# Optimization experiments

Hardware: AMD Instinct MI355X
Metric: run time of the kernel (lower is better)

The kernel has to match this reference:

```python
import jax, jax.numpy as jnp
import numpy as np

D = 128
K = 8
TEMPERATURE = 1.0
LN_EPS = 1e-5
NORM_EPS = 1e-12


def setup_inputs() -> dict:
    key = jax.random.key(0)
    ks = jax.random.split(key, 6)
    B = 262144
    global_prosody = jax.random.normal(ks[0], (B, D), dtype=jnp.float32)
    W = jax.random.normal(ks[1], (D, D), dtype=jnp.float32) / np.sqrt(D)
    b = jnp.zeros((D,), dtype=jnp.float32)
    gamma = jnp.ones((D,), dtype=jnp.float32)
    beta = jnp.zeros((D,), dtype=jnp.float32)
    # codebook initialized as rows of an orthonormal basis (SVD of random init)
    init = jax.random.normal(ks[2], (D, K), dtype=jnp.float32)
    U, _, _ = jnp.linalg.svd(init, full_matrices=False)
    codebook = U[:, :K].T  # (K, D)
    return {"global_prosody": global_prosody, "W": W, "b": b,
            "gamma": gamma, "beta": beta, "codebook": codebook}


def _l2norm(x, axis=-1):
    n = jnp.sqrt(jnp.sum(x * x, axis=axis, keepdims=True))
    return x / jnp.maximum(n, NORM_EPS)


def reference(global_prosody, W, b, gamma, beta, codebook):
    # proj: Linear + LayerNorm
    h = global_prosody @ W.T + b                      # (B, D)
    mu = jnp.mean(h, axis=-1, keepdims=True)
    var = jnp.var(h, axis=-1, keepdims=True)
    h = (h - mu) / jnp.sqrt(var + LN_EPS) * gamma + beta
    # cosine-sim logits
    h_norm = _l2norm(h)                               # (B, D)
    cb_norm = _l2norm(codebook)                       # (K, D)
    logits = (h_norm @ cb_norm.T) / TEMPERATURE       # (B, K)
    soft_assign = jax.nn.softmax(logits, axis=-1)
    hard_indices = jnp.argmax(logits, axis=-1)        # (B,)
    hard_assign = jax.nn.one_hot(hard_indices, K, dtype=jnp.float32)
    # straight-through assignment
    assign = hard_assign + soft_assign - jax.lax.stop_gradient(soft_assign)
    embedding = assign @ codebook                     # (B, D)
    return hard_indices, soft_assign, embedding, logits
```

## Files before the change

### kernel.cpp

```cpp
#include <hip/hip_runtime.h>
#include <math.h>

#define DD 128
#define KK 8
#define LN_EPS 1e-5f
#define NORM_EPS 1e-12f

typedef __attribute__((ext_vector_type(8))) short bf16x8;
typedef __attribute__((ext_vector_type(16))) float f32x16;
typedef unsigned int uint;
typedef unsigned short ushort;

#define G2B_OFF_F   (122880 / 4)
#define SCAL_OFF_F  (123904 / 4)

__device__ inline void split3(float x, uint& h, uint& m, uint& l) {
    uint u0 = __float_as_uint(x);
    uint rh = (u0 + 0x7FFFu + ((u0 >> 16) & 1u)) & 0xFFFF0000u;
    float xh = __uint_as_float(rh);
    float r1 = x - xh;
    uint u1 = __float_as_uint(r1);
    uint rm = (u1 + 0x7FFFu + ((u1 >> 16) & 1u)) & 0xFFFF0000u;
    float xm = __uint_as_float(rm);
    float r2 = r1 - xm;
    uint u2 = __float_as_uint(r2);
    uint rl = (u2 + 0x7FFFu + ((u2 >> 16) & 1u));
    h = rh; m = rm; l = rl;
}

__device__ inline void split3t(float x, uint& h, uint& m, uint& l) {
    uint u0 = __float_as_uint(x);
    float xh = __uint_as_float(u0 & 0xFFFF0000u);
    float r1 = x - xh;
    uint u1 = __float_as_uint(r1);
    float xm = __uint_as_float(u1 & 0xFFFF0000u);
    float r2 = r1 - xm;
    h = u0; m = u1; l = __float_as_uint(r2);
}

__device__ inline uint packhi(uint a1, uint a0) {
    return __builtin_amdgcn_perm(a1, a0, 0x07060302u);
}

__device__ inline void split2packt(float e0, float e1, uint& ph, uint& pm, uint& pl) {
    uint h0, m0, l0, h1, m1, l1;
    split3t(e0, h0, m0, l0);
    split3t(e1, h1, m1, l1);
    ph = packhi(h1, h0);
    pm = packhi(m1, m0);
    pl = packhi(l1, l0);
}

union FragU  { uint4 u; bf16x8 f; };
union AccU16 { f32x16 v; float a[16]; };

__global__ void l1q_prep0(const float* __restrict__ b, const float* __restrict__ gamma,
                          const float* __restrict__ beta, const float* __restrict__ cb,
                          float* __restrict__ ws)
{
    __shared__ float invn_s[KK];
    const int t = threadIdx.x;
    if (t < KK) {
        float s = 0.f;
        for (int j = 0; j < DD; ++j) { float v = cb[t * DD + j]; s = fmaf(v, v, s); }
        invn_s[t] = 1.0f / fmaxf(sqrtf(s), NORM_EPS);
    }
    __syncthreads();
    {
        float g = gamma[t];
        float* g2b = ws + G2B_OFF_F;
        g2b[2 * t]     = g * g;
        g2b[2 * t + 1] = b[t];
    }
    float* scal = ws + SCAL_OFF_F;
    if (t < KK) {
        float in = invn_s[t];
        float p = 0.f, q = 0.f, cu = 0.f;
        for (int j = 0; j < DD; ++j) {
            float c = cb[t * DD + j] * in;
            p  = fmaf(c, gamma[j], p);
            q  = fmaf(c, beta[j], q);
            cu = fmaf(c * gamma[j], b[j], cu);
        }
        scal[t]      = p;
        scal[8 + t]  = q;
        scal[22 + t] = cu;
    }
    if (t == 16) { float s = 0.f; for (int j = 0; j < DD; ++j) { float g = gamma[j]; s = fmaf(g, g, s); } scal[16] = s; }
    if (t == 17) { float s = 0.f; for (int j = 0; j < DD; ++j) s = fmaf(gamma[j], beta[j], s); scal[17] = s; }
    if (t == 18) { float s = 0.f; for (int j = 0; j < DD; ++j) { float v = beta[j]; s = fmaf(v, v, s); } scal[18] = s; }
    if (t == 19) { float s = 0.f; for (int j = 0; j < DD; ++j) s += b[j]; scal[19] = s; }
    if (t == 20) { float s = 0.f; for (int j = 0; j < DD; ++j) s = fmaf(gamma[j] * gamma[j], b[j], s); scal[20] = s; }
    if (t == 21) { float s = 0.f; for (int j = 0; j < DD; ++j) s = fmaf(gamma[j] * beta[j], b[j], s); scal[21] = s; }
}

__global__ void l1q_prepA(const float* __restrict__ W, const float* __restrict__ b,
                          const float* __restrict__ gamma, const float* __restrict__ beta,
                          const float* __restrict__ cb, ushort* __restrict__ wsA)
{
    __shared__ float invn_s[KK];
    __shared__ float we[11][DD];
    __shared__ float wext[32][16];
    const int t = threadIdx.x;
    const int jt = blockIdx.x >> 3;
    const int ks = blockIdx.x & 7;

    if (jt == 4) {
        if (t < KK) {
            float s = 0.f;
            for (int j = 0; j < DD; ++j) { float v = cb[t * DD + j]; s = fmaf(v, v, s); }
            invn_s[t] = 1.0f / fmaxf(sqrtf(s), NORM_EPS);
        }
        __syncthreads();
        for (int idx = t; idx < 11 * DD; idx += 256) {
            int e = idx / DD, j = idx % DD;
            float g = gamma[j];
            float v;
            if (e == 0)      v = 1.0f;
            else if (e == 1) v = g * g;
            else if (e == 2) v = g * beta[j];
            else             v = cb[(e - 3) * DD + j] * invn_s[e - 3] * g;
            we[e][j] = v;
        }
        __syncthreads();
    }

    for (int idx = t; idx < 512; idx += 256) {
        int jl = idx >> 4, kk = idx & 15;
        int k = ks * 16 + kk;
        float val;
        if (jt < 4) {
            val = W[(jt * 32 + jl) * DD + k];
        } else if (jl < 11) {
            float s = 0.f;
            for (int j = 0; j < DD; ++j) s = fmaf(we[jl][j], W[j * DD + k], s);
            val = s;
        } else {
            val = 0.f;
        }
        wext[jl][kk] = val;
    }
    __syncthreads();

    for (int idx = t; idx < 512; idx += 256) {
        int jl = idx >> 4, kk = idx & 15;
        int lane = jl + 32 * (kk >> 3);
        int i = kk & 7;
        uint h, m, l;
        split3(wext[jl][kk], h, m, l);
        int base = jt * 8 + ks;
        wsA[(0 * 40 + base) * 512 + lane * 8 + i] = (ushort)(h >> 16);
        wsA[(1 * 40 + base) * 512 + lane * 8 + i] = (ushort)(m >> 16);
        wsA[(2 * 40 + base) * 512 + lane * 8 + i] = (ushort)(l >> 16);
    }
}

__global__ __launch_bounds__(1024, 4)
void l1q_main(const float* __restrict__ x, const ushort* __restrict__ wsA,
              const float* __restrict__ wsf, const float* __restrict__ cb,
              float* __restrict__ out_idx, float* __restrict__ out_soft,
              float* __restrict__ out_emb, float* __restrict__ out_log,
              int B)
{
    __shared__ uint4 Wl4[7680];
    __shared__ float gath[16][352];
    __shared__ int   besti[16][32];
    __shared__ float g2b_s[256];
    __shared__ float scal_s[32];

    const int t = threadIdx.x;
    const int wave = t >> 6;
    const int lane = t & 63;
    const int n = lane & 31;
    const int h = lane >> 5;

    const float* xp = x + (size_t)(blockIdx.x * 1024 + wave * 32 + n) * DD + h * 8;
    float4 ra = *(const float4*)(xp + 0);
    float4 rc = *(const float4*)(xp + 4);

    {
        const uint4* src = (const uint4*)wsA;
        #pragma unroll
        for (int i = 0; i < 8; ++i) {
            int idx = t + i * 1024;
            if (idx < 7680) Wl4[idx] = src[idx];
        }
    }
    if (t < 256) g2b_s[t] = wsf[G2B_OFF_F + t];
    if (t < 32)  scal_s[t] = wsf[SCAL_OFF_F + t];
    __syncthreads();

    const float inv128 = 1.0f / 128.0f;

    #pragma unroll 1
    for (int c = 0; c < 2; ++c) {
        const int rowbase = blockIdx.x * 1024 + c * 512 + wave * 32;
        const float* xnext = (c == 0) ? (xp + 512 * DD) : xp;

        f32x16 acc[5];
        #pragma unroll
        for (int jt = 0; jt < 5; ++jt)
            #pragma unroll
            for (int r = 0; r < 16; ++r) acc[jt][r] = 0.f;

        #pragma unroll
        for (int ks = 0; ks < 8; ++ks) {
            const float* pf = (ks < 7) ? (xp + (ks + 1) * 16) : xnext;
            float4 na = *(const float4*)(pf + 0);
            float4 nc = *(const float4*)(pf + 4);

            FragU xh, xm, xl;
            split2packt(ra.x, ra.y, xh.u.x, xm.u.x, xl.u.x);
            split2packt(ra.z, ra.w, xh.u.y, xm.u.y, xl.u.y);
            split2packt(rc.x, rc.y, xh.u.z, xm.u.z, xl.u.z);
            split2packt(rc.z, rc.w, xh.u.w, xm.u.w, xl.u.w);

            __builtin_amdgcn_s_setprio(1);
            #pragma unroll
            for (int jt = 0; jt < 5; ++jt) {
                const int pl = jt * 8 + ks;
                FragU wh, wm, wl;
                wh.u = Wl4[(0 * 40 + pl) * 64 + lane];
                wm.u = Wl4[(1 * 40 + pl) * 64 + lane];
                wl.u = Wl4[(2 * 40 + pl) * 64 + lane];
                f32x16 cacc = acc[jt];
                cacc = __builtin_amdgcn_mfma_f32_32x32x16_bf16(wl.f, xh.f, cacc, 0, 0, 0);
                cacc = __builtin_amdgcn_mfma_f32_32x32x16_bf16(wh.f, xl.f, cacc, 0, 0, 0);
                cacc = __builtin_amdgcn_mfma_f32_32x32x16_bf16(wm.f, xm.f, cacc, 0, 0, 0);
                cacc = __builtin_amdgcn_mfma_f32_32x32x16_bf16(wm.f, xh.f, cacc, 0, 0, 0);
                cacc = __builtin_amdgcn_mfma_f32_32x32x16_bf16(wh.f, xm.f, cacc, 0, 0, 0);
                cacc = __builtin_amdgcn_mfma_f32_32x32x16_bf16(wh.f, xh.f, cacc, 0, 0, 0);
                acc[jt] = cacc;
            }
            __builtin_amdgcn_s_setprio(0);
            ra = na; rc = nc;
        }

        float s2a = 0.f, t2a = 0.f;
        #pragma unroll
        for (int jt = 0; jt < 4; ++jt) {
            AccU16 a; a.v = acc[jt];
            #pragma unroll
            for (int rq = 0; rq < 4; ++rq) {
                int jb = jt * 32 + 8 * rq + 4 * h;
                #pragma unroll
                for (int r = 0; r < 4; ++r) {
                    float2 gb = *(const float2*)&g2b_s[2 * (jb + r)];
                    float hv = a.a[rq * 4 + r] + gb.y;
                    float h2 = hv * hv;
                    s2a += h2;
                    t2a = fmaf(gb.x, h2, t2a);
                }
            }
        }
        s2a += __shfl_xor(s2a, 32);
        t2a += __shfl_xor(t2a, 32);

        {
            AccU16 a; a.v = acc[4];
            #pragma unroll
            for (int rq = 0; rq < 4; ++rq) {
                #pragma unroll
                for (int r = 0; r < 4; ++r) {
                    int local = r + 8 * rq + 4 * h;
                    if (local < 11) gath[wave][n * 11 + local] = a.a[rq * 4 + r];
                }
            }
        }
        __builtin_amdgcn_s_waitcnt(0);
        const float* gp = &gath[wave][n * 11];

        const float cg2s = scal_s[16], cgbs = scal_s[17], cb2s = scal_s[18];

        float s1  = gp[0] + scal_s[19];
        float t1  = gp[1] + scal_s[20];
        float r1v = gp[2] + scal_s[21];
        float u[KK];
        #pragma unroll
        for (int k = 0; k < KK; ++k) u[k] = gp[3 + k] + scal_s[22 + k];

        float mu = s1 * inv128;
        float var = fmaf(-mu, mu, s2a * inv128);
        float istd = 1.0f / sqrtf(var + LN_EPS);
        float nrm2 = istd * istd * (t2a - 2.f * mu * t1 + mu * mu * cg2s)
                   + 2.f * istd * (r1v - mu * cgbs) + cb2s;
        float rinv = 1.0f / fmaxf(sqrtf(fmaxf(nrm2, 0.f)), NORM_EPS);

        float lg[KK];
        #pragma unroll
        for (int k = 0; k < KK; ++k)
            lg[k] = (istd * (u[k] - mu * scal_s[k]) + scal_s[8 + k]) * rinv;

        float mx = lg[0]; int bi = 0;
        #pragma unroll
        for (int k = 1; k < KK; ++k) if (lg[k] > mx) { mx = lg[k]; bi = k; }

        float ex[KK], se = 0.f;
        #pragma unroll
        for (int k = 0; k < KK; ++k) { ex[k] = expf(lg[k] - mx); se += ex[k]; }
        float rse = 1.0f / se;

        const int m = rowbase + n;
        if (h == 0) {
            out_idx[m] = (float)bi;
            besti[wave][n] = bi;
            *(float4*)&out_log[(size_t)m * KK]     = make_float4(lg[0], lg[1], lg[2], lg[3]);
            *(float4*)&out_log[(size_t)m * KK + 4] = make_float4(lg[4], lg[5], lg[6], lg[7]);
        } else {
            *(float4*)&out_soft[(size_t)m * KK]     = make_float4(ex[0] * rse, ex[1] * rse, ex[2] * rse, ex[3] * rse);
            *(float4*)&out_soft[(size_t)m * KK + 4] = make_float4(ex[4] * rse, ex[5] * rse, ex[6] * rse, ex[7] * rse);
        }

        __builtin_amdgcn_s_waitcnt(0);
        const float4* cb4 = (const float4*)cb;
        float4* eo = (float4*)out_emb;
        #pragma unroll
        for (int i = 0; i < 16; ++i) {
            int f4 = lane + 64 * i;
            int rl = f4 >> 5;
            int cc = f4 & 31;
            int k0 = besti[wave][rl];
            eo[(size_t)(rowbase + rl) * 32 + cc] = cb4[k0 * 32 + cc];
        }

        xp = xnext;
    }
}

extern "C" void kernel_launch(void* const* d_in, const int* in_sizes, int n_in,
                              void* d_out, int out_size, void* d_ws, size_t ws_size,
                              hipStream_t stream) {
    const float* x     = (const float*)d_in[0];
    const float* W     = (const float*)d_in[1];
    const float* b     = (const float*)d_in[2];
    const float* gamma = (const float*)d_in[3];
    const float* beta  = (const float*)d_in[4];
    const float* cb    = (const float*)d_in[5];
    const int B = in_sizes[0] / DD;

    float*  ws  = (float*)d_ws;
    ushort* wsA = (ushort*)d_ws;

    float* out    = (float*)d_out;
    float* o_idx  = out;
    float* o_soft = out + (size_t)B;
    float* o_emb  = out + (size_t)B * (1 + KK);
    float* o_log  = out + (size_t)B * (1 + KK + DD);

    hipLaunchKernelGGL(l1q_prep0, dim3(1), dim3(128), 0, stream, b, gamma, beta, cb, ws);
    hipLaunchKernelGGL(l1q_prepA, dim3(40), dim3(256), 0, stream, W, b, gamma, beta, cb, wsA);
    const int grid = B / 1024;
    hipLaunchKernelGGL(l1q_main, dim3(grid), dim3(1024), 0, stream,
                       x, wsA, ws, cb, o_idx, o_soft, o_emb, o_log, B);
}
```

Measured before the change: 308.3 us.

## Preload whole row of x into registers and overlap next chunk load with epilogue

Instead of a one-step-ahead prefetch inside the k-loop, each thread now loads all eight x fragments for its row up front, and issues the second chunk's loads right after the first chunk's MFMA loop so they overlap the LayerNorm/softmax/store epilogue. The full s_waitcnt(0) calls are replaced with an lgkm-only wait so outstanding global loads are not drained at the LDS barriers, and the s_setprio hints are removed. This raises register pressure by 64 VGPRs for the buffered fragments, which may reduce occupancy.

```diff
diff --git a/kernel.cpp b/kernel.cpp
--- a/kernel.cpp
+++ b/kernel.cpp
@@ -175,8 +175,6 @@
     const int h = lane >> 5;
 
     const float* xp = x + (size_t)(blockIdx.x * 1024 + wave * 32 + n) * DD + h * 8;
-    float4 ra = *(const float4*)(xp + 0);
-    float4 rc = *(const float4*)(xp + 4);
 
     {
         const uint4* src = (const uint4*)wsA;
@@ -190,12 +188,18 @@
     if (t < 32)  scal_s[t] = wsf[SCAL_OFF_F + t];
     __syncthreads();
 
+    float4 xa[8], xc[8];
+    #pragma unroll
+    for (int ks = 0; ks < 8; ++ks) {
+        xa[ks] = *(const float4*)(xp + ks * 16);
+        xc[ks] = *(const float4*)(xp + ks * 16 + 4);
+    }
+
     const float inv128 = 1.0f / 128.0f;
 
     #pragma unroll 1
     for (int c = 0; c < 2; ++c) {
         const int rowbase = blockIdx.x * 1024 + c * 512 + wave * 32;
-        const float* xnext = (c == 0) ? (xp + 512 * DD) : xp;
 
         f32x16 acc[5];
         #pragma unroll
@@ -205,17 +209,12 @@
 
         #pragma unroll
         for (int ks = 0; ks < 8; ++ks) {
-            const float* pf = (ks < 7) ? (xp + (ks + 1) * 16) : xnext;
-            float4 na = *(const float4*)(pf + 0);
-            float4 nc = *(const float4*)(pf + 4);
-
             FragU xh, xm, xl;
-            split2packt(ra.x, ra.y, xh.u.x, xm.u.x, xl.u.x);
-            split2packt(ra.z, ra.w, xh.u.y, xm.u.y, xl.u.y);
-            split2packt(rc.x, rc.y, xh.u.z, xm.u.z, xl.u.z);
-            split2packt(rc.z, rc.w, xh.u.w, xm.u.w, xl.u.w);
-
-            __builtin_amdgcn_s_setprio(1);
+            split2packt(xa[ks].x, xa[ks].y, xh.u.x, xm.u.x, xl.u.x);
+            split2packt(xa[ks].z, xa[ks].w, xh.u.y, xm.u.y, xl.u.y);
+            split2packt(xc[ks].x, xc[ks].y, xh.u.z, xm.u.z, xl.u.z);
+            split2packt(xc[ks].z, xc[ks].w, xh.u.w, xm.u.w, xl.u.w);
+
             #pragma unroll
             for (int jt = 0; jt < 5; ++jt) {
                 const int pl = jt * 8 + ks;
@@ -232,8 +231,15 @@
                 cacc = __builtin_amdgcn_mfma_f32_32x32x16_bf16(wh.f, xh.f, cacc, 0, 0, 0);
                 acc[jt] = cacc;
             }
-            __builtin_amdgcn_s_setprio(0);
-            ra = na; rc = nc;
+        }
+
+        if (c == 0) {
+            const float* xq = xp + 512 * DD;
+            #pragma unroll
+            for (int ks = 0; ks < 8; ++ks) {
+                xa[ks] = *(const float4*)(xq + ks * 16);
+                xc[ks] = *(const float4*)(xq + ks * 16 + 4);
+            }
         }
 
         float s2a = 0.f, t2a = 0.f;
@@ -267,7 +273,7 @@
                 }
             }
         }
-        __builtin_amdgcn_s_waitcnt(0);
+        __builtin_amdgcn_s_waitcnt(0xc07f);
         const float* gp = &gath[wave][n * 11];
 
         const float cg2s = scal_s[16], cgbs = scal_s[17], cb2s = scal_s[18];
@@ -311,7 +317,7 @@
             *(float4*)&out_soft[(size_t)m * KK + 4] = make_float4(ex[4] * rse, ex[5] * rse, ex[6] * rse, ex[7] * rse);
         }
 
-        __builtin_amdgcn_s_waitcnt(0);
+        __builtin_amdgcn_s_waitcnt(0xc07f);
         const float4* cb4 = (const float4*)cb;
         float4* eo = (float4*)out_emb;
         #pragma unroll
@@ -322,8 +328,6 @@
             int k0 = besti[wave][rl];
             eo[(size_t)(rowbase + rl) * 32 + cc] = cb4[k0 * 32 + cc];
         }
-
-        xp = xnext;
     }
 }
 
```

Result: slower. 354.0 us (+14.8%).
